# Kernel tuning notes

Measured on AMD Instinct MI355X. Metric: run time of the kernel, lower is better.

## Reference

```python
import jax, jax.numpy as jnp
import numpy as np
import math

E = 1024   # embedding_dim
H = 16     # num_attention_heads
DH = 64    # head_embedding_dim
THD = H * DH
EPS = 1e-5

def _layernorm(x, g, b):
    m = jnp.mean(x, axis=-1, keepdims=True)
    v = jnp.mean(jnp.square(x - m), axis=-1, keepdims=True)
    return (x - m) * jax.lax.rsqrt(v + EPS) * g + b

def setup_inputs() -> dict:
    key = jax.random.key(0)
    ks = jax.random.split(key, 16)
    s_in = 1.0 / math.sqrt(E)
    s_o = 1.0 / math.sqrt(THD)
    inp = {"tokens": jax.random.normal(ks[0], (2, 2048, E), dtype=jnp.float32)}
    # q_linear / k_linear / v_linear: LayerNorm(E) then Linear(E -> THD)
    for i, name in enumerate(["q", "k", "v"]):
        inp[f"ln_{name}_g"] = jnp.ones((E,), jnp.float32)
        inp[f"ln_{name}_b"] = jnp.zeros((E,), jnp.float32)
        inp[f"W{name}"] = jax.random.uniform(ks[1 + 2 * i], (E, THD), jnp.float32, -s_in, s_in)
        inp[f"b{name}"] = jax.random.uniform(ks[2 + 2 * i], (THD,), jnp.float32, -s_in, s_in)
    # attention_linear: LayerNorm(THD) then Linear(THD -> E)
    inp["ln_o_g"] = jnp.ones((THD,), jnp.float32)
    inp["ln_o_b"] = jnp.zeros((THD,), jnp.float32)
    inp["Wo"] = jax.random.uniform(ks[7], (THD, E), jnp.float32, -s_o, s_o)
    inp["bo"] = jax.random.uniform(ks[8], (E,), jnp.float32, -s_o, s_o)
    return inp

def reference(tokens, ln_q_g, ln_q_b, Wq, bq, ln_k_g, ln_k_b, Wk, bk,
              ln_v_g, ln_v_b, Wv, bv, ln_o_g, ln_o_b, Wo, bo):
    N, L, _ = tokens.shape
    # NOTE: faithful to source quirk -- k comes from v_linear, v comes from k_linear.
    q = (_layernorm(tokens, ln_q_g, ln_q_b) @ Wq + bq).reshape(N, L, H, DH).transpose(0, 2, 1, 3)  # (N,H,L,Dh)
    k = (_layernorm(tokens, ln_v_g, ln_v_b) @ Wv + bv).reshape(N, L, H, DH).transpose(0, 2, 3, 1)  # (N,H,Dh,L)
    v = (_layernorm(tokens, ln_k_g, ln_k_b) @ Wk + bk).reshape(N, L, H, DH).transpose(0, 2, 1, 3)  # (N,H,L,Dh)
    qkT = jnp.einsum('bhid,bhdj->bhij', q, k)  # (N,H,L,L)
    # mask added BEFORE dividing by sqrt(Dh), as in source
    mask = jnp.triu(jnp.full((L, L), -9999.0, dtype=qkT.dtype), k=1)
    attn = jax.nn.softmax((qkT + mask) / math.sqrt(DH), axis=-1)
    wv = jnp.einsum('bhij,bhjd->bhid', attn, v).transpose(0, 2, 1, 3).reshape(N, L, THD)
    out = _layernorm(wv, ln_o_g, ln_o_b) @ Wo + bo + tokens
    return (out, k, v)
```

## Files before the change

kernel.cpp:

```cpp
#include <hip/hip_runtime.h>

#define L_SEQ 2048
#define NH    16
#define E_DIM 1024
#define M_ROWS 4096

typedef unsigned short u16;
typedef unsigned int   u32;
typedef __attribute__((ext_vector_type(8))) __bf16 bf16x8;
typedef __attribute__((ext_vector_type(4))) float  f32x4;

__device__ __forceinline__ u16 f2bf(float f) {
  union { float f; u32 u; } x; x.f = f;
  u32 u = x.u;
  return (u16)((u + 0x7FFFu + ((u >> 16) & 1u)) >> 16);
}
__device__ __forceinline__ float bf2f(u16 v) {
  union { u32 u; float f; } x; x.u = ((u32)v) << 16;
  return x.f;
}
__device__ __forceinline__ void st_bf4(u16* p, float a, float b, float c, float d) {
  ushort4 u; u.x = f2bf(a); u.y = f2bf(b); u.z = f2bf(c); u.w = f2bf(d);
  *reinterpret_cast<ushort4*>(p) = u;
}
__device__ __forceinline__ void gload16(const u16* g, u16* l) {
  __builtin_amdgcn_global_load_lds(
      (const __attribute__((address_space(1))) void*)g,
      (__attribute__((address_space(3))) void*)l, 16, 0, 0);
}
#define SBAR() asm volatile("s_barrier" ::: "memory")

__global__ __launch_bounds__(256) void ln_hat_f32(const float* __restrict__ x, u16* __restrict__ o)
{
  __shared__ float red[8];
  const size_t row = blockIdx.x;
  const int t = threadIdx.x;
  float4 v = reinterpret_cast<const float4*>(x + row * E_DIM)[t];
  float s = v.x + v.y + v.z + v.w;
  float q = v.x*v.x + v.y*v.y + v.z*v.z + v.w*v.w;
  #pragma unroll
  for (int off = 32; off; off >>= 1) { s += __shfl_down(s, off); q += __shfl_down(q, off); }
  if ((t & 63) == 0) { red[t >> 6] = s; red[4 + (t >> 6)] = q; }
  __syncthreads();
  float S = red[0] + red[1] + red[2] + red[3];
  float Q = red[4] + red[5] + red[6] + red[7];
  float mean = S * (1.f / E_DIM);
  float rstd = rsqrtf(Q * (1.f / E_DIM) - mean * mean + 1e-5f);
  st_bf4(o + row * E_DIM + t * 4,
         (v.x - mean) * rstd, (v.y - mean) * rstd, (v.z - mean) * rstd, (v.w - mean) * rstd);
}

__global__ __launch_bounds__(256) void ln_hat_bf16(const u16* __restrict__ x, u16* __restrict__ o)
{
  __shared__ float red[8];
  const size_t row = blockIdx.x;
  const int t = threadIdx.x;
  ushort4 u = reinterpret_cast<const ushort4*>(x + row * E_DIM)[t];
  float v0 = bf2f(u.x), v1 = bf2f(u.y), v2 = bf2f(u.z), v3 = bf2f(u.w);
  float s = v0 + v1 + v2 + v3;
  float q = v0*v0 + v1*v1 + v2*v2 + v3*v3;
  #pragma unroll
  for (int off = 32; off; off >>= 1) { s += __shfl_down(s, off); q += __shfl_down(q, off); }
  if ((t & 63) == 0) { red[t >> 6] = s; red[4 + (t >> 6)] = q; }
  __syncthreads();
  float S = red[0] + red[1] + red[2] + red[3];
  float Q = red[4] + red[5] + red[6] + red[7];
  float mean = S * (1.f / E_DIM);
  float rstd = rsqrtf(Q * (1.f / E_DIM) - mean * mean + 1e-5f);
  st_bf4(o + row * E_DIM + t * 4,
         (v0 - mean) * rstd, (v1 - mean) * rstd, (v2 - mean) * rstd, (v3 - mean) * rstd);
}

__global__ __launch_bounds__(256) void transpose_all(
    const float* __restrict__ W0, const float* __restrict__ W1,
    const float* __restrict__ W2, const float* __restrict__ W3,
    const float* __restrict__ g0, const float* __restrict__ g1,
    const float* __restrict__ g2, const float* __restrict__ g3,
    u16* __restrict__ T0, u16* __restrict__ T1, u16* __restrict__ T2, u16* __restrict__ T3)
{
  __shared__ float tile[32][33];
  const int z = blockIdx.z;
  const float* W = (z == 0) ? W0 : (z == 1) ? W1 : (z == 2) ? W2 : W3;
  const float* g = (z == 0) ? g0 : (z == 1) ? g1 : (z == 2) ? g2 : g3;
  u16* T = (z == 0) ? T0 : (z == 1) ? T1 : (z == 2) ? T2 : T3;
  const int tx = threadIdx.x & 31, ty = threadIdx.x >> 5;
  const int bx = blockIdx.x * 32, by = blockIdx.y * 32;
  #pragma unroll
  for (int r = 0; r < 4; ++r) {
    const int e = by + ty + r * 8;
    tile[ty + r * 8][tx] = W[(size_t)e * E_DIM + bx + tx] * g[e];
  }
  __syncthreads();
  #pragma unroll
  for (int r = 0; r < 4; ++r)
    T[(size_t)(bx + ty + r * 8) * E_DIM + by + tx] = f2bf(tile[tx][ty + r * 8]);
}

__global__ __launch_bounds__(256) void bias_fold(
    const float* __restrict__ W0, const float* __restrict__ W1,
    const float* __restrict__ W2, const float* __restrict__ W3,
    const float* __restrict__ l0, const float* __restrict__ l1,
    const float* __restrict__ l2, const float* __restrict__ l3,
    const float* __restrict__ b0, const float* __restrict__ b1,
    const float* __restrict__ b2, const float* __restrict__ b3,
    float* __restrict__ bfold)
{
  __shared__ float part[8][32];
  const int z = blockIdx.y;
  const float* W  = (z == 0) ? W0 : (z == 1) ? W1 : (z == 2) ? W2 : W3;
  const float* bl = (z == 0) ? l0 : (z == 1) ? l1 : (z == 2) ? l2 : l3;
  const float* bs = (z == 0) ? b0 : (z == 1) ? b1 : (z == 2) ? b2 : b3;
  const int tn = threadIdx.x & 31, te = threadIdx.x >> 5;
  const int n = blockIdx.x * 32 + tn;
  float acc = 0.f;
  const int e0 = te * 128;
  for (int e = e0; e < e0 + 128; ++e) acc += bl[e] * W[(size_t)e * E_DIM + n];
  part[te][tn] = acc;
  __syncthreads();
  if (te == 0) {
    float s = part[0][tn] + part[1][tn] + part[2][tn] + part[3][tn]
            + part[4][tn] + part[5][tn] + part[6][tn] + part[7][tn];
    bfold[z * E_DIM + n] = bs[n] + s;
  }
}

#define GBK 64
__device__ __forceinline__ void core128(
    const u16* __restrict__ A, const u16* __restrict__ BT,
    int m0, int n0, int t, u16* lds, f32x4 (&acc)[4][4])
{
  const int lane = t & 63, wave = t >> 6;
  const int wm = wave >> 1, wn = wave & 1;
  const int fr = lane & 15, hi = lane >> 4;
  const int sx = fr & 7;

  auto STAGE = [&](int buf, int kt) {
    u16* la = lds + (buf * 2 + 0) * (128 * GBK);
    u16* lb = lds + (buf * 2 + 1) * (128 * GBK);
    #pragma unroll
    for (int s = 0; s < 4; ++s) {
      const int seg = t + s * 256;
      const int r = seg >> 3;
      const int gc = (seg & 7) ^ (r & 7);
      gload16(A + (size_t)(m0 + r) * E_DIM + kt * GBK + gc * 8, la + seg * 8);
    }
    #pragma unroll
    for (int s = 0; s < 4; ++s) {
      const int seg = t + s * 256;
      const int r = seg >> 3;
      const int gc = (seg & 7) ^ (r & 7);
      gload16(BT + (size_t)(n0 + r) * E_DIM + kt * GBK + gc * 8, lb + seg * 8);
    }
  };
  auto AF = [&](int buf, int i, int ks) -> bf16x8 {
    return *reinterpret_cast<const bf16x8*>(
        lds + (buf * 2 + 0) * (128 * GBK) + (wm * 64 + i * 16 + fr) * GBK + (((ks * 4 + hi) ^ sx) * 8));
  };
  auto BF = [&](int buf, int j, int ks) -> bf16x8 {
    return *reinterpret_cast<const bf16x8*>(
        lds + (buf * 2 + 1) * (128 * GBK) + (wn * 64 + j * 16 + fr) * GBK + (((ks * 4 + hi) ^ sx) * 8));
  };
  auto PHASES = [&](int buf) {
    bf16x8 a[4][2], b[4][2];
    #pragma unroll
    for (int i = 0; i < 4; ++i) { a[i][0] = AF(buf, i, 0); a[i][1] = AF(buf, i, 1); }
    #pragma unroll
    for (int j = 0; j < 4; ++j) { b[j][0] = BF(buf, j, 0); b[j][1] = BF(buf, j, 1); }
    __builtin_amdgcn_s_setprio(1);
    #pragma unroll
    for (int i = 0; i < 4; ++i)
      #pragma unroll
      for (int j = 0; j < 4; ++j) {
        acc[i][j] = __builtin_amdgcn_mfma_f32_16x16x32_bf16(a[i][0], b[j][0], acc[i][j], 0, 0, 0);
        acc[i][j] = __builtin_amdgcn_mfma_f32_16x16x32_bf16(a[i][1], b[j][1], acc[i][j], 0, 0, 0);
      }
    __builtin_amdgcn_s_setprio(0);
  };

  STAGE(0, 0);
  #pragma unroll 1
  for (int kt = 0; kt < 15; ++kt) {
    const int buf = kt & 1;
    SBAR();
    STAGE(buf ^ 1, kt + 1);
    asm volatile("s_waitcnt vmcnt(8)" ::: "memory");
    SBAR();
    PHASES(buf);
  }
  asm volatile("s_waitcnt vmcnt(0)" ::: "memory");
  SBAR();
  PHASES(1);
}

__global__ __launch_bounds__(256, 2) void gemm_qkv128(
    const u16* __restrict__ xhat, const u16* __restrict__ WTcat,
    const float* __restrict__ bfold,
    float* __restrict__ kout, float* __restrict__ vout,
    u16* __restrict__ qbf, u16* __restrict__ kbf, u16* __restrict__ vTb)
{
  __shared__ __align__(16) char smraw[128 * 132 * 4];
  u16* lds = (u16*)smraw;
  const int t = threadIdx.x;
  const int xcd = blockIdx.x & 7, l = blockIdx.x >> 3;
  const int by = 8 * (xcd >> 1) + l / 12;
  const int bx = 12 * (xcd & 1) + l % 12;
  const int m0 = by * 128, n0 = bx * 128;

  f32x4 acc[4][4] = {};
  core128(xhat, WTcat, m0, n0, t, lds, acc);

  const int lane = t & 63, wave = t >> 6;
  const int wm = wave >> 1, wn = wave & 1;
  const int fr = lane & 15, hi = lane >> 4;
  const int z = n0 >> 10;
  const float* bias = bfold + z * E_DIM;
  const int rowb = hi * 4;
  const int bb = m0 >> 11;

  if (z == 0) {
    #pragma unroll
    for (int i = 0; i < 4; ++i) {
      const int mbase = m0 + wm * 64 + i * 16 + rowb;
      #pragma unroll
      for (int j = 0; j < 4; ++j) {
        const int ncol = (n0 + wn * 64 + j * 16 + fr) & 1023;
        const float bval = bias[ncol];
        const int h = ncol >> 6, d = ncol & 63;
        #pragma unroll
        for (int r = 0; r < 4; ++r) {
          const int m = mbase + r;
          const int ltok = m & 2047;
          qbf[(((size_t)(bb * NH + h) * L_SEQ + ltok) << 6) + d] = f2bf(acc[i][j][r] + bval);
        }
      }
    }
  } else if (z == 1) {
    __syncthreads();
    float (*xp)[132] = (float(*)[132])smraw;
    #pragma unroll
    for (int i = 0; i < 4; ++i) {
      const int mbase = m0 + wm * 64 + i * 16 + rowb;
      const int mloc = wm * 64 + i * 16 + rowb;
      #pragma unroll
      for (int j = 0; j < 4; ++j) {
        const int nl = wn * 64 + j * 16 + fr;
        const int ncol = (n0 + nl) & 1023;
        const float bval = bias[ncol];
        const int h = ncol >> 6, d = ncol & 63;
        #pragma unroll
        for (int r = 0; r < 4; ++r) {
          const int m = mbase + r;
          const int ltok = m & 2047;
          const float val = acc[i][j][r] + bval;
          kbf[(((size_t)(bb * NH + h) * L_SEQ + ltok) << 6) + d] = f2bf(val);
          xp[nl][mloc + r] = val;
        }
      }
    }
    __syncthreads();
    const int nl = t >> 1, mh = (t & 1) * 64;
    const int ncol2 = (n0 + nl) & 1023;
    const int h2 = ncol2 >> 6, d2 = ncol2 & 63;
    float4* dst = (float4*)(kout + ((size_t)(bb * NH + h2) * 64 + d2) * L_SEQ + (m0 & 2047) + mh);
    #pragma unroll
    for (int u = 0; u < 16; ++u)
      dst[u] = *reinterpret_cast<float4*>(&xp[nl][mh + u * 4]);
  } else {
    __syncthreads();
    u32 (*vp)[68] = (u32(*)[68])smraw;
    #pragma unroll
    for (int i = 0; i < 4; ++i) {
      const int mbase = m0 + wm * 64 + i * 16 + rowb;
      const int mloc = wm * 64 + i * 16 + rowb;
      #pragma unroll
      for (int j = 0; j < 4; ++j) {
        const int nl = wn * 64 + j * 16 + fr;
        const int ncol = (n0 + nl) & 1023;
        const float bval = bias[ncol];
        const int h = ncol >> 6, d = ncol & 63;
        float v4[4];
        #pragma unroll
        for (int r = 0; r < 4; ++r) {
          const int m = mbase + r;
          const int ltok = m & 2047;
          v4[r] = acc[i][j][r] + bval;
          vout[((size_t)(bb * NH + h) * L_SEQ + ltok) * 64 + d] = v4[r];
        }
        vp[nl][(mloc >> 1) + 0] = (u32)f2bf(v4[0]) | ((u32)f2bf(v4[1]) << 16);
        vp[nl][(mloc >> 1) + 1] = (u32)f2bf(v4[2]) | ((u32)f2bf(v4[3]) << 16);
      }
    }
    __syncthreads();
    const int nl = t >> 1, mh = (t & 1) * 64;
    const int ncol2 = (n0 + nl) & 1023;
    const int h2 = ncol2 >> 6, d2 = ncol2 & 63;
    uint4* dst = (uint4*)(vTb + ((size_t)(bb * NH + h2) * 64 + d2) * L_SEQ + (m0 & 2047) + mh);
    #pragma unroll
    for (int u = 0; u < 8; ++u)
      dst[u] = *reinterpret_cast<uint4*>(&vp[nl][(mh >> 1) + u * 4]);
  }
}

__global__ __launch_bounds__(256, 2) void gemm_o128(
    const u16* __restrict__ A, const u16* __restrict__ BT, const float* __restrict__ bias,
    const float* __restrict__ tokens, float* __restrict__ out)
{
  __shared__ u16 lds[4 * 128 * GBK];
  const int t = threadIdx.x;
  const int xcd = blockIdx.x & 7, l = blockIdx.x >> 3;
  const int by = 8 * (xcd >> 1) + (l >> 2);
  const int bx = 4 * (xcd & 1) + (l & 3);
  const int m0 = by * 128, n0 = bx * 128;

  f32x4 acc[4][4] = {};
  core128(A, BT, m0, n0, t, lds, acc);

  const int lane = t & 63, wave = t >> 6;
  const int wm = wave >> 1, wn = wave & 1;
  const int fr = lane & 15, hi = lane >> 4;
  const int rowb = hi * 4;
  #pragma unroll
  for (int i = 0; i < 4; ++i) {
    const int mbase = m0 + wm * 64 + i * 16 + rowb;
    #pragma unroll
    for (int j = 0; j < 4; ++j) {
      const int ncol = n0 + wn * 64 + j * 16 + fr;
      const float bval = bias[ncol];
      #pragma unroll
      for (int r = 0; r < 4; ++r) {
        const int m = mbase + r;
        out[(size_t)m * E_DIM + ncol] = acc[i][j][r] + bval + tokens[(size_t)m * E_DIM + ncol];
      }
    }
  }
}

__global__ __launch_bounds__(256) void attn_mfma(
    const u16* __restrict__ qbf, const u16* __restrict__ kbf,
    const u16* __restrict__ vTb, u16* __restrict__ wv)
{
  __shared__ u16 Klds[64][72];
  __shared__ u16 Vlds[64][72];
  __shared__ u16 Plds[4][16][72];
  const int t = threadIdx.x, lane = t & 63, wave = t >> 6;
  const int bi = blockIdx.x;
  const int bh = (bi & 7) + 8 * ((bi >> 3) & 3);
  const int pr = bi >> 5;
  const int fr = lane & 15, hi = lane >> 4;
  const u16* kbase = kbf + (size_t)bh * L_SEQ * 64;
  const u16* vbase = vTb + (size_t)bh * 64 * L_SEQ;
  const int b = bh >> 4, h = bh & 15;

  #pragma unroll 1
  for (int half = 0; half < 2; ++half) {
    const int qt = half ? (31 - pr) : pr;
    const int q0w = qt * 64 + wave * 16;
    const int qg = q0w + fr;

    const u16* qrow = qbf + ((size_t)bh * L_SEQ + q0w + fr) * 64 + hi * 8;
    const bf16x8 qf0 = *reinterpret_cast<const bf16x8*>(qrow);
    const bf16x8 qf1 = *reinterpret_cast<const bf16x8*>(qrow + 32);

    f32x4 o[4] = {};
    float mrun = -3.0e38f, lrun = 0.f;

    for (int tkv = 0; tkv <= qt; ++tkv) {
      const int j0 = tkv * 64;
      const bool diag = (tkv == qt);
      #pragma unroll
      for (int s = 0; s < 2; ++s) {
        const int seg = t + s * 256;
        const int r = seg >> 3, c8 = (seg & 7) * 8;
        *reinterpret_cast<uint4*>(&Klds[r][c8]) =
            *reinterpret_cast<const uint4*>(kbase + (size_t)(j0 + r) * 64 + c8);
        *reinterpret_cast<uint4*>(&Vlds[r][c8]) =
            *reinterpret_cast<const uint4*>(vbase + (size_t)r * L_SEQ + j0 + c8);
      }
      __syncthreads();

      f32x4 st[4] = {};
      __builtin_amdgcn_s_setprio(1);
      #pragma unroll
      for (int kt = 0; kt < 4; ++kt) {
        bf16x8 ka0 = *reinterpret_cast<const bf16x8*>(&Klds[kt*16 + fr][hi*8]);
        bf16x8 ka1 = *reinterpret_cast<const bf16x8*>(&Klds[kt*16 + fr][32 + hi*8]);
        st[kt] = __builtin_amdgcn_mfma_f32_16x16x32_bf16(ka0, qf0, st[kt], 0, 0, 0);
        st[kt] = __builtin_amdgcn_mfma_f32_16x16x32_bf16(ka1, qf1, st[kt], 0, 0, 0);
      }
      __builtin_amdgcn_s_setprio(0);

      float p[16];
      float pmax = -3.0e38f;
      #pragma unroll
      for (int kt = 0; kt < 4; ++kt)
        #pragma unroll
        for (int r = 0; r < 4; ++r) {
          const int key = j0 + kt*16 + hi*4 + r;
          const float v = st[kt][r] * 0.125f +
                          ((diag && key > qg) ? -1249.875f : 0.f);
          p[kt*4 + r] = v;
          pmax = fmaxf(pmax, v);
        }
      pmax = fmaxf(pmax, __shfl_xor(pmax, 16));
      pmax = fmaxf(pmax, __shfl_xor(pmax, 32));
      const float mnew = fmaxf(mrun, pmax);
      const float alpha = __expf(mrun - mnew);
      float lsum = 0.f;
      #pragma unroll
      for (int i = 0; i < 16; ++i) { p[i] = __expf(p[i] - mnew); lsum += p[i]; }
      lsum += __shfl_xor(lsum, 16);
      lsum += __shfl_xor(lsum, 32);
      lrun = lrun * alpha + lsum;
      mrun = mnew;
      #pragma unroll
      for (int r = 0; r < 4; ++r) {
        const float ar = __shfl(alpha, hi*4 + r);
        o[0][r] *= ar; o[1][r] *= ar; o[2][r] *= ar; o[3][r] *= ar;
      }

      #pragma unroll
      for (int kt = 0; kt < 4; ++kt) {
        ushort4 w4;
        w4.x = f2bf(p[kt*4+0]); w4.y = f2bf(p[kt*4+1]);
        w4.z = f2bf(p[kt*4+2]); w4.w = f2bf(p[kt*4+3]);
        *reinterpret_cast<ushort4*>(&Plds[wave][fr][kt*16 + hi*4]) = w4;
      }

      const bf16x8 pf0 = *reinterpret_cast<const bf16x8*>(&Plds[wave][fr][hi*8]);
      const bf16x8 pf1 = *reinterpret_cast<const bf16x8*>(&Plds[wave][fr][32 + hi*8]);
      __builtin_amdgcn_s_setprio(1);
      #pragma unroll
      for (int dt = 0; dt < 4; ++dt) {
        bf16x8 vf0 = *reinterpret_cast<const bf16x8*>(&Vlds[dt*16 + fr][hi*8]);
        bf16x8 vf1 = *reinterpret_cast<const bf16x8*>(&Vlds[dt*16 + fr][32 + hi*8]);
        o[dt] = __builtin_amdgcn_mfma_f32_16x16x32_bf16(pf0, vf0, o[dt], 0, 0, 0);
        o[dt] = __builtin_amdgcn_mfma_f32_16x16x32_bf16(pf1, vf1, o[dt], 0, 0, 0);
      }
      __builtin_amdgcn_s_setprio(0);
      __syncthreads();
    }

    const float inv = 1.f / lrun;
    #pragma unroll
    for (int r = 0; r < 4; ++r) {
      const float ir = __shfl(inv, hi*4 + r);
      const int q = q0w + hi*4 + r;
      u16* dst = wv + (size_t)(b * L_SEQ + q) * E_DIM + h * 64 + fr;
      #pragma unroll
      for (int dt = 0; dt < 4; ++dt)
        dst[dt * 16] = f2bf(o[dt][r] * ir);
    }
  }
}

extern "C" void kernel_launch(void* const* d_in, const int* in_sizes, int n_in,
                              void* d_out, int out_size, void* d_ws, size_t ws_size,
                              hipStream_t stream) {
  (void)in_sizes; (void)n_in; (void)out_size; (void)ws_size;
  const float* tokens = (const float*)d_in[0];
  const float* ln_q_g = (const float*)d_in[1];
  const float* ln_q_b = (const float*)d_in[2];
  const float* Wq     = (const float*)d_in[3];
  const float* bq     = (const float*)d_in[4];
  const float* ln_k_g = (const float*)d_in[5];
  const float* ln_k_b = (const float*)d_in[6];
  const float* Wk     = (const float*)d_in[7];
  const float* bk     = (const float*)d_in[8];
  const float* ln_v_g = (const float*)d_in[9];
  const float* ln_v_b = (const float*)d_in[10];
  const float* Wv     = (const float*)d_in[11];
  const float* bv     = (const float*)d_in[12];
  const float* ln_o_g = (const float*)d_in[13];
  const float* ln_o_b = (const float*)d_in[14];
  const float* Wo     = (const float*)d_in[15];
  const float* bo     = (const float*)d_in[16];

  float* out  = (float*)d_out;
  float* kout = out + 4194304;
  float* vout = kout + 4194304;

  char* w = (char*)d_ws;
  const size_t MB = (size_t)1 << 20;
  u16*   WTq   = (u16*)(w + 0 * MB);
  u16*   WTv   = (u16*)(w + 2 * MB);
  u16*   WTk   = (u16*)(w + 4 * MB);
  u16*   WTo   = (u16*)(w + 6 * MB);
  u16*   xhat  = (u16*)(w + 8 * MB);
  u16*   qbf   = (u16*)(w + 16 * MB);
  u16*   kbf   = (u16*)(w + 24 * MB);
  u16*   vTb   = (u16*)(w + 32 * MB);
  u16*   what  = (u16*)(w + 40 * MB);
  float* bfold = (float*)(w + 48 * MB);
  u16*   wvb   = xhat;

  transpose_all<<<dim3(32, 32, 4), 256, 0, stream>>>(
      Wq, Wv, Wk, Wo, ln_q_g, ln_v_g, ln_k_g, ln_o_g, WTq, WTv, WTk, WTo);
  bias_fold<<<dim3(32, 4), 256, 0, stream>>>(
      Wq, Wv, Wk, Wo, ln_q_b, ln_v_b, ln_k_b, ln_o_b, bq, bv, bk, bo, bfold);
  ln_hat_f32<<<M_ROWS, 256, 0, stream>>>(tokens, xhat);
  gemm_qkv128<<<768, 256, 0, stream>>>(xhat, WTq, bfold, kout, vout, qbf, kbf, vTb);
  attn_mfma<<<512, 256, 0, stream>>>(qbf, kbf, vTb, wvb);
  ln_hat_bf16<<<M_ROWS, 256, 0, stream>>>(wvb, what);
  gemm_o128<<<256, 256, 0, stream>>>(what, WTo, bfold + 3 * E_DIM, tokens, out);
}
```

Measured before the change: 129.8 us.

## Split causal attention KV range across two blocks and merge partials

Adds a split-KV attention kernel that launches twice as many blocks. Each pair of blocks shares the long query tile's KV range: one block covers tiles 0-16, the other covers the rest and then also handles the short query tile. Partial outputs plus running max and sum go to workspace and are merged by a new combine kernel. The aim is better load balance and more occupancy on the many-CU device, at the cost of an extra launch and fp32 partial traffic. It runs only when the workspace is large enough.

```diff
diff --git a/kernel.cpp b/kernel.cpp
--- a/kernel.cpp
+++ b/kernel.cpp
@@ -335,6 +335,183 @@
   }
 }
 
+__global__ __launch_bounds__(256, 4) void attn_split(
+    const u16* __restrict__ qbf, const u16* __restrict__ kbf,
+    const u16* __restrict__ vTb, u16* __restrict__ wv,
+    float* __restrict__ po, float* __restrict__ pml)
+{
+  __shared__ u16 Klds[64][72];
+  __shared__ u16 Vlds[64][72];
+  __shared__ u16 Plds[4][16][72];
+  const int t = threadIdx.x, lane = t & 63, wave = t >> 6;
+  const int bi = blockIdx.x;
+  const int bh = (bi & 7) + 8 * ((bi >> 3) & 3);
+  const int pp = bi >> 5;
+  const int half = pp & 1, pr = pp >> 1;
+  const int fr = lane & 15, hi = lane >> 4;
+  const u16* kbase = kbf + (size_t)bh * L_SEQ * 64;
+  const u16* vbase = vTb + (size_t)bh * 64 * L_SEQ;
+  const int b = bh >> 4, h = bh & 15;
+  const int qtA = 31 - pr, qtB = pr;
+
+  auto STG = [&](int j0) {
+    #pragma unroll
+    for (int s = 0; s < 2; ++s) {
+      const int seg = t + s * 256;
+      const int r = seg >> 3, c8 = (seg & 7) * 8;
+      *reinterpret_cast<uint4*>(&Klds[r][c8]) =
+          *reinterpret_cast<const uint4*>(kbase + (size_t)(j0 + r) * 64 + c8);
+      *reinterpret_cast<uint4*>(&Vlds[r][c8]) =
+          *reinterpret_cast<const uint4*>(vbase + (size_t)r * L_SEQ + j0 + c8);
+    }
+  };
+  auto TILE = [&](const bf16x8& qf0, const bf16x8& qf1, int qg, bool diag, int j0,
+                  f32x4 (&o)[4], float& mrun, float& lrun) {
+    f32x4 st[4] = {};
+    __builtin_amdgcn_s_setprio(1);
+    #pragma unroll
+    for (int kt = 0; kt < 4; ++kt) {
+      bf16x8 ka0 = *reinterpret_cast<const bf16x8*>(&Klds[kt*16 + fr][hi*8]);
+      bf16x8 ka1 = *reinterpret_cast<const bf16x8*>(&Klds[kt*16 + fr][32 + hi*8]);
+      st[kt] = __builtin_amdgcn_mfma_f32_16x16x32_bf16(ka0, qf0, st[kt], 0, 0, 0);
+      st[kt] = __builtin_amdgcn_mfma_f32_16x16x32_bf16(ka1, qf1, st[kt], 0, 0, 0);
+    }
+    __builtin_amdgcn_s_setprio(0);
+
+    float p[16];
+    float pmax = -3.0e38f;
+    #pragma unroll
+    for (int kt = 0; kt < 4; ++kt)
+      #pragma unroll
+      for (int r = 0; r < 4; ++r) {
+        const int key = j0 + kt*16 + hi*4 + r;
+        const float v = st[kt][r] * 0.125f + ((diag && key > qg) ? -1249.875f : 0.f);
+        p[kt*4 + r] = v;
+        pmax = fmaxf(pmax, v);
+      }
+    pmax = fmaxf(pmax, __shfl_xor(pmax, 16));
+    pmax = fmaxf(pmax, __shfl_xor(pmax, 32));
+    const float mnew = fmaxf(mrun, pmax);
+    const float alpha = __expf(mrun - mnew);
+    float lsum = 0.f;
+    #pragma unroll
+    for (int i = 0; i < 16; ++i) { p[i] = __expf(p[i] - mnew); lsum += p[i]; }
+    lsum += __shfl_xor(lsum, 16);
+    lsum += __shfl_xor(lsum, 32);
+    lrun = lrun * alpha + lsum;
+    mrun = mnew;
+    #pragma unroll
+    for (int r = 0; r < 4; ++r) {
+      const float ar = __shfl(alpha, hi*4 + r);
+      o[0][r] *= ar; o[1][r] *= ar; o[2][r] *= ar; o[3][r] *= ar;
+    }
+    #pragma unroll
+    for (int kt = 0; kt < 4; ++kt) {
+      ushort4 w4;
+      w4.x = f2bf(p[kt*4+0]); w4.y = f2bf(p[kt*4+1]);
+      w4.z = f2bf(p[kt*4+2]); w4.w = f2bf(p[kt*4+3]);
+      *reinterpret_cast<ushort4*>(&Plds[wave][fr][kt*16 + hi*4]) = w4;
+    }
+    const bf16x8 pf0 = *reinterpret_cast<const bf16x8*>(&Plds[wave][fr][hi*8]);
+    const bf16x8 pf1 = *reinterpret_cast<const bf16x8*>(&Plds[wave][fr][32 + hi*8]);
+    __builtin_amdgcn_s_setprio(1);
+    #pragma unroll
+    for (int dt = 0; dt < 4; ++dt) {
+      bf16x8 vf0 = *reinterpret_cast<const bf16x8*>(&Vlds[dt*16 + fr][hi*8]);
+      bf16x8 vf1 = *reinterpret_cast<const bf16x8*>(&Vlds[dt*16 + fr][32 + hi*8]);
+      o[dt] = __builtin_amdgcn_mfma_f32_16x16x32_bf16(pf0, vf0, o[dt], 0, 0, 0);
+      o[dt] = __builtin_amdgcn_mfma_f32_16x16x32_bf16(pf1, vf1, o[dt], 0, 0, 0);
+    }
+    __builtin_amdgcn_s_setprio(0);
+  };
+
+  {
+    const int q0w = qtA * 64 + wave * 16;
+    const int qg = q0w + fr;
+    const u16* qrow = qbf + ((size_t)bh * L_SEQ + q0w + fr) * 64 + hi * 8;
+    const bf16x8 qf0 = *reinterpret_cast<const bf16x8*>(qrow);
+    const bf16x8 qf1 = *reinterpret_cast<const bf16x8*>(qrow + 32);
+    f32x4 o[4] = {};
+    float mrun = -3.0e38f, lrun = 0.f;
+    const int lo = half ? 17 : 0;
+    const int hiT = half ? qtA : 16;
+    #pragma unroll 1
+    for (int tkv = lo; tkv <= hiT; ++tkv) {
+      STG(tkv * 64);
+      __syncthreads();
+      TILE(qf0, qf1, qg, tkv == qtA, tkv * 64, o, mrun, lrun);
+      __syncthreads();
+    }
+    const int slot = (bh * 16 + pr) * 2 + half;
+    float* pob = po + (size_t)slot * 4096;
+    #pragma unroll
+    for (int dt = 0; dt < 4; ++dt)
+      #pragma unroll
+      for (int r = 0; r < 4; ++r)
+        pob[(wave * 16 + hi * 4 + r) * 64 + dt * 16 + fr] = o[dt][r];
+    if (hi == 0) {
+      pml[slot * 128 + wave * 16 + fr] = mrun;
+      pml[slot * 128 + 64 + wave * 16 + fr] = lrun;
+    }
+  }
+
+  if (half) {
+    const int q0w = qtB * 64 + wave * 16;
+    const int qg = q0w + fr;
+    const u16* qrow = qbf + ((size_t)bh * L_SEQ + q0w + fr) * 64 + hi * 8;
+    const bf16x8 qf0 = *reinterpret_cast<const bf16x8*>(qrow);
+    const bf16x8 qf1 = *reinterpret_cast<const bf16x8*>(qrow + 32);
+    f32x4 o[4] = {};
+    float mrun = -3.0e38f, lrun = 0.f;
+    #pragma unroll 1
+    for (int tkv = 0; tkv <= qtB; ++tkv) {
+      __syncthreads();
+      STG(tkv * 64);
+      __syncthreads();
+      TILE(qf0, qf1, qg, tkv == qtB, tkv * 64, o, mrun, lrun);
+    }
+    const float inv = 1.f / lrun;
+    #pragma unroll
+    for (int r = 0; r < 4; ++r) {
+      const float ir = __shfl(inv, hi * 4 + r);
+      const int q = q0w + hi * 4 + r;
+      u16* dst = wv + (size_t)(b * L_SEQ + q) * E_DIM + h * 64 + fr;
+      #pragma unroll
+      for (int dt = 0; dt < 4; ++dt)
+        dst[dt * 16] = f2bf(o[dt][r] * ir);
+    }
+  }
+}
+
+__global__ __launch_bounds__(256) void attn_combine(
+    const float* __restrict__ po, const float* __restrict__ pml, u16* __restrict__ wv)
+{
+  const int pair = blockIdx.x;
+  const int bh = pair >> 4, pr = pair & 15;
+  const int b = bh >> 4, h = bh & 15;
+  const int q0 = (31 - pr) * 64;
+  const int t = threadIdx.x;
+  const int r = t >> 2, c0 = (t & 3) * 16;
+  const float m0 = pml[(size_t)(pair * 2 + 0) * 128 + r];
+  const float l0 = pml[(size_t)(pair * 2 + 0) * 128 + 64 + r];
+  const float m1 = pml[(size_t)(pair * 2 + 1) * 128 + r];
+  const float l1 = pml[(size_t)(pair * 2 + 1) * 128 + 64 + r];
+  const float mm = fmaxf(m0, m1);
+  const float a0 = __expf(m0 - mm), a1 = __expf(m1 - mm);
+  const float inv = 1.f / (l0 * a0 + l1 * a1);
+  const float* o0 = po + ((size_t)(pair * 2 + 0) * 64 + r) * 64 + c0;
+  const float* o1 = po + ((size_t)(pair * 2 + 1) * 64 + r) * 64 + c0;
+  u16* dst = wv + (size_t)(b * L_SEQ + q0 + r) * E_DIM + h * 64 + c0;
+  #pragma unroll
+  for (int c = 0; c < 16; c += 4) {
+    float4 x0 = *reinterpret_cast<const float4*>(o0 + c);
+    float4 x1 = *reinterpret_cast<const float4*>(o1 + c);
+    st_bf4(dst + c,
+           (x0.x * a0 + x1.x * a1) * inv, (x0.y * a0 + x1.y * a1) * inv,
+           (x0.z * a0 + x1.z * a1) * inv, (x0.w * a0 + x1.w * a1) * inv);
+  }
+}
+
 __global__ __launch_bounds__(256) void attn_mfma(
     const u16* __restrict__ qbf, const u16* __restrict__ kbf,
     const u16* __restrict__ vTb, u16* __restrict__ wv)
@@ -356,11 +533,9 @@
     const int qt = half ? (31 - pr) : pr;
     const int q0w = qt * 64 + wave * 16;
     const int qg = q0w + fr;
-
     const u16* qrow = qbf + ((size_t)bh * L_SEQ + q0w + fr) * 64 + hi * 8;
     const bf16x8 qf0 = *reinterpret_cast<const bf16x8*>(qrow);
     const bf16x8 qf1 = *reinterpret_cast<const bf16x8*>(qrow + 32);
-
     f32x4 o[4] = {};
     float mrun = -3.0e38f, lrun = 0.f;
 
@@ -396,8 +571,7 @@
         #pragma unroll
         for (int r = 0; r < 4; ++r) {
           const int key = j0 + kt*16 + hi*4 + r;
-          const float v = st[kt][r] * 0.125f +
-                          ((diag && key > qg) ? -1249.875f : 0.f);
+          const float v = st[kt][r] * 0.125f + ((diag && key > qg) ? -1249.875f : 0.f);
           p[kt*4 + r] = v;
           pmax = fmaxf(pmax, v);
         }
@@ -417,7 +591,6 @@
         const float ar = __shfl(alpha, hi*4 + r);
         o[0][r] *= ar; o[1][r] *= ar; o[2][r] *= ar; o[3][r] *= ar;
       }
-
       #pragma unroll
       for (int kt = 0; kt < 4; ++kt) {
         ushort4 w4;
@@ -425,7 +598,6 @@
         w4.z = f2bf(p[kt*4+2]); w4.w = f2bf(p[kt*4+3]);
         *reinterpret_cast<ushort4*>(&Plds[wave][fr][kt*16 + hi*4]) = w4;
       }
-
       const bf16x8 pf0 = *reinterpret_cast<const bf16x8*>(&Plds[wave][fr][hi*8]);
       const bf16x8 pf1 = *reinterpret_cast<const bf16x8*>(&Plds[wave][fr][32 + hi*8]);
       __builtin_amdgcn_s_setprio(1);
@@ -456,7 +628,7 @@
 extern "C" void kernel_launch(void* const* d_in, const int* in_sizes, int n_in,
                               void* d_out, int out_size, void* d_ws, size_t ws_size,
                               hipStream_t stream) {
-  (void)in_sizes; (void)n_in; (void)out_size; (void)ws_size;
+  (void)in_sizes; (void)n_in; (void)out_size;
   const float* tokens = (const float*)d_in[0];
   const float* ln_q_g = (const float*)d_in[1];
   const float* ln_q_b = (const float*)d_in[2];
@@ -491,6 +663,8 @@
   u16*   vTb   = (u16*)(w + 32 * MB);
   u16*   what  = (u16*)(w + 40 * MB);
   float* bfold = (float*)(w + 48 * MB);
+  float* po    = (float*)(w + 49 * MB);
+  float* pml   = (float*)(w + 65 * MB);
   u16*   wvb   = xhat;
 
   transpose_all<<<dim3(32, 32, 4), 256, 0, stream>>>(
@@ -499,7 +673,12 @@
       Wq, Wv, Wk, Wo, ln_q_b, ln_v_b, ln_k_b, ln_o_b, bq, bv, bk, bo, bfold);
   ln_hat_f32<<<M_ROWS, 256, 0, stream>>>(tokens, xhat);
   gemm_qkv128<<<768, 256, 0, stream>>>(xhat, WTq, bfold, kout, vout, qbf, kbf, vTb);
-  attn_mfma<<<512, 256, 0, stream>>>(qbf, kbf, vTb, wvb);
+  if (ws_size >= 66 * MB) {
+    attn_split<<<1024, 256, 0, stream>>>(qbf, kbf, vTb, wvb, po, pml);
+    attn_combine<<<512, 256, 0, stream>>>(po, pml, wvb);
+  } else {
+    attn_mfma<<<512, 256, 0, stream>>>(qbf, kbf, vTb, wvb);
+  }
   ln_hat_bf16<<<M_ROWS, 256, 0, stream>>>(wvb, what);
   gemm_o128<<<256, 256, 0, stream>>>(what, WTo, bfold + 3 * E_DIM, tokens, out);
 }
```

Result: no change. 129.5 us (-0.2%).

## Split long attention rows across blocks, read K/V directly, fuse prep kernels

Applied to the files above, without the earlier changes.

Fuses the weight transpose, bias fold and input layernorm into one prep kernel launch. Attention now splits the long causal query tiles across two blocks (split-KV), writing fp32 partial outputs plus running max and sum, and the output layernorm kernel merges them. The attention kernel drops its shared-memory K/V staging and loads MFMA fragments straight from global memory, with no per-tile barriers and a 4-block occupancy hint. The aim is better load balance, more parallelism and fewer launches, at the cost of extra partial-result traffic and uncoalesced, unshared global K/V reads.

```diff
diff --git a/kernel.cpp b/kernel.cpp
--- a/kernel.cpp
+++ b/kernel.cpp
@@ -30,33 +30,112 @@
 }
 #define SBAR() asm volatile("s_barrier" ::: "memory")
 
-__global__ __launch_bounds__(256) void ln_hat_f32(const float* __restrict__ x, u16* __restrict__ o)
+__global__ __launch_bounds__(256) void prep_kernel(
+    const float* __restrict__ tokens,
+    const float* __restrict__ W0, const float* __restrict__ W1,
+    const float* __restrict__ W2, const float* __restrict__ W3,
+    const float* __restrict__ g0, const float* __restrict__ g1,
+    const float* __restrict__ g2, const float* __restrict__ g3,
+    const float* __restrict__ lb0, const float* __restrict__ lb1,
+    const float* __restrict__ lb2, const float* __restrict__ lb3,
+    const float* __restrict__ bs0, const float* __restrict__ bs1,
+    const float* __restrict__ bs2, const float* __restrict__ bs3,
+    u16* __restrict__ T0, u16* __restrict__ T1, u16* __restrict__ T2, u16* __restrict__ T3,
+    float* __restrict__ bfold, u16* __restrict__ xhat)
+{
+  __shared__ __align__(16) float shm[32 * 33];
+  const int bid = blockIdx.x;
+  const int t = threadIdx.x;
+
+  if (bid < 4096) {
+    const int z = bid >> 10, rem = bid & 1023;
+    const float* W = (z == 0) ? W0 : (z == 1) ? W1 : (z == 2) ? W2 : W3;
+    const float* g = (z == 0) ? g0 : (z == 1) ? g1 : (z == 2) ? g2 : g3;
+    u16* T = (z == 0) ? T0 : (z == 1) ? T1 : (z == 2) ? T2 : T3;
+    float (*tile)[33] = (float(*)[33])shm;
+    const int tx = t & 31, ty = t >> 5;
+    const int bx = (rem & 31) * 32, by = (rem >> 5) * 32;
+    #pragma unroll
+    for (int r = 0; r < 4; ++r) {
+      const int e = by + ty + r * 8;
+      tile[ty + r * 8][tx] = W[(size_t)e * E_DIM + bx + tx] * g[e];
+    }
+    __syncthreads();
+    #pragma unroll
+    for (int r = 0; r < 4; ++r)
+      T[(size_t)(bx + ty + r * 8) * E_DIM + by + tx] = f2bf(tile[tx][ty + r * 8]);
+  } else if (bid < 4224) {
+    const int idx = bid - 4096;
+    const int z = idx >> 5;
+    const float* W  = (z == 0) ? W0 : (z == 1) ? W1 : (z == 2) ? W2 : W3;
+    const float* bl = (z == 0) ? lb0 : (z == 1) ? lb1 : (z == 2) ? lb2 : lb3;
+    const float* bs = (z == 0) ? bs0 : (z == 1) ? bs1 : (z == 2) ? bs2 : bs3;
+    float (*part)[32] = (float(*)[32])shm;
+    const int tn = t & 31, te = t >> 5;
+    const int n = (idx & 31) * 32 + tn;
+    float acc = 0.f;
+    const int e0 = te * 128;
+    for (int e = e0; e < e0 + 128; ++e) acc += bl[e] * W[(size_t)e * E_DIM + n];
+    part[te][tn] = acc;
+    __syncthreads();
+    if (te == 0) {
+      float s = part[0][tn] + part[1][tn] + part[2][tn] + part[3][tn]
+              + part[4][tn] + part[5][tn] + part[6][tn] + part[7][tn];
+      bfold[z * E_DIM + n] = bs[n] + s;
+    }
+  } else {
+    float* red = shm;
+    const size_t row = bid - 4224;
+    float4 v = reinterpret_cast<const float4*>(tokens + row * E_DIM)[t];
+    float s = v.x + v.y + v.z + v.w;
+    float q = v.x*v.x + v.y*v.y + v.z*v.z + v.w*v.w;
+    #pragma unroll
+    for (int off = 32; off; off >>= 1) { s += __shfl_down(s, off); q += __shfl_down(q, off); }
+    if ((t & 63) == 0) { red[t >> 6] = s; red[4 + (t >> 6)] = q; }
+    __syncthreads();
+    float S = red[0] + red[1] + red[2] + red[3];
+    float Q = red[4] + red[5] + red[6] + red[7];
+    float mean = S * (1.f / E_DIM);
+    float rstd = rsqrtf(Q * (1.f / E_DIM) - mean * mean + 1e-5f);
+    st_bf4(xhat + row * E_DIM + t * 4,
+           (v.x - mean) * rstd, (v.y - mean) * rstd, (v.z - mean) * rstd, (v.w - mean) * rstd);
+  }
+}
+
+__global__ __launch_bounds__(256) void ln_combine_hat(
+    const u16* __restrict__ wvb, const float* __restrict__ po,
+    const float* __restrict__ pml, u16* __restrict__ what)
 {
   __shared__ float red[8];
-  const size_t row = blockIdx.x;
+  const int row = blockIdx.x;
   const int t = threadIdx.x;
-  float4 v = reinterpret_cast<const float4*>(x + row * E_DIM)[t];
-  float s = v.x + v.y + v.z + v.w;
-  float q = v.x*v.x + v.y*v.y + v.z*v.z + v.w*v.w;
-  #pragma unroll
-  for (int off = 32; off; off >>= 1) { s += __shfl_down(s, off); q += __shfl_down(q, off); }
-  if ((t & 63) == 0) { red[t >> 6] = s; red[4 + (t >> 6)] = q; }
-  __syncthreads();
-  float S = red[0] + red[1] + red[2] + red[3];
-  float Q = red[4] + red[5] + red[6] + red[7];
-  float mean = S * (1.f / E_DIM);
-  float rstd = rsqrtf(Q * (1.f / E_DIM) - mean * mean + 1e-5f);
-  st_bf4(o + row * E_DIM + t * 4,
-         (v.x - mean) * rstd, (v.y - mean) * rstd, (v.z - mean) * rstd, (v.w - mean) * rstd);
-}
-
-__global__ __launch_bounds__(256) void ln_hat_bf16(const u16* __restrict__ x, u16* __restrict__ o)
-{
-  __shared__ float red[8];
-  const size_t row = blockIdx.x;
-  const int t = threadIdx.x;
-  ushort4 u = reinterpret_cast<const ushort4*>(x + row * E_DIM)[t];
-  float v0 = bf2f(u.x), v1 = bf2f(u.y), v2 = bf2f(u.z), v3 = bf2f(u.w);
+  const int l = row & (L_SEQ - 1), b = row >> 11;
+  const int qt = l >> 6;
+  float v0, v1, v2, v3;
+  if (qt >= 16) {
+    const int pr = 31 - qt;
+    const int c = t * 4;
+    const int h = c >> 6, d0 = c & 63;
+    const int bh = b * NH + h;
+    const int base = (bh * 16 + pr) * 2;
+    const int rr = l & 63;
+    const float m0 = pml[(size_t)base * 128 + rr];
+    const float s0 = pml[(size_t)base * 128 + 64 + rr];
+    const float m1 = pml[(size_t)(base + 1) * 128 + rr];
+    const float s1 = pml[(size_t)(base + 1) * 128 + 64 + rr];
+    const float mm = fmaxf(m0, m1);
+    const float a0 = __expf(m0 - mm), a1 = __expf(m1 - mm);
+    const float inv = 1.f / (s0 * a0 + s1 * a1);
+    float4 x0 = *reinterpret_cast<const float4*>(po + ((size_t)base * 64 + rr) * 64 + d0);
+    float4 x1 = *reinterpret_cast<const float4*>(po + ((size_t)(base + 1) * 64 + rr) * 64 + d0);
+    v0 = (x0.x * a0 + x1.x * a1) * inv;
+    v1 = (x0.y * a0 + x1.y * a1) * inv;
+    v2 = (x0.z * a0 + x1.z * a1) * inv;
+    v3 = (x0.w * a0 + x1.w * a1) * inv;
+  } else {
+    ushort4 u = reinterpret_cast<const ushort4*>(wvb + (size_t)row * E_DIM)[t];
+    v0 = bf2f(u.x); v1 = bf2f(u.y); v2 = bf2f(u.z); v3 = bf2f(u.w);
+  }
   float s = v0 + v1 + v2 + v3;
   float q = v0*v0 + v1*v1 + v2*v2 + v3*v3;
   #pragma unroll
@@ -67,61 +146,8 @@
   float Q = red[4] + red[5] + red[6] + red[7];
   float mean = S * (1.f / E_DIM);
   float rstd = rsqrtf(Q * (1.f / E_DIM) - mean * mean + 1e-5f);
-  st_bf4(o + row * E_DIM + t * 4,
+  st_bf4(what + (size_t)row * E_DIM + t * 4,
          (v0 - mean) * rstd, (v1 - mean) * rstd, (v2 - mean) * rstd, (v3 - mean) * rstd);
-}
-
-__global__ __launch_bounds__(256) void transpose_all(
-    const float* __restrict__ W0, const float* __restrict__ W1,
-    const float* __restrict__ W2, const float* __restrict__ W3,
-    const float* __restrict__ g0, const float* __restrict__ g1,
-    const float* __restrict__ g2, const float* __restrict__ g3,
-    u16* __restrict__ T0, u16* __restrict__ T1, u16* __restrict__ T2, u16* __restrict__ T3)
-{
-  __shared__ float tile[32][33];
-  const int z = blockIdx.z;
-  const float* W = (z == 0) ? W0 : (z == 1) ? W1 : (z == 2) ? W2 : W3;
-  const float* g = (z == 0) ? g0 : (z == 1) ? g1 : (z == 2) ? g2 : g3;
-  u16* T = (z == 0) ? T0 : (z == 1) ? T1 : (z == 2) ? T2 : T3;
-  const int tx = threadIdx.x & 31, ty = threadIdx.x >> 5;
-  const int bx = blockIdx.x * 32, by = blockIdx.y * 32;
-  #pragma unroll
-  for (int r = 0; r < 4; ++r) {
-    const int e = by + ty + r * 8;
-    tile[ty + r * 8][tx] = W[(size_t)e * E_DIM + bx + tx] * g[e];
-  }
-  __syncthreads();
-  #pragma unroll
-  for (int r = 0; r < 4; ++r)
-    T[(size_t)(bx + ty + r * 8) * E_DIM + by + tx] = f2bf(tile[tx][ty + r * 8]);
-}
-
-__global__ __launch_bounds__(256) void bias_fold(
-    const float* __restrict__ W0, const float* __restrict__ W1,
-    const float* __restrict__ W2, const float* __restrict__ W3,
-    const float* __restrict__ l0, const float* __restrict__ l1,
-    const float* __restrict__ l2, const float* __restrict__ l3,
-    const float* __restrict__ b0, const float* __restrict__ b1,
-    const float* __restrict__ b2, const float* __restrict__ b3,
-    float* __restrict__ bfold)
-{
-  __shared__ float part[8][32];
-  const int z = blockIdx.y;
-  const float* W  = (z == 0) ? W0 : (z == 1) ? W1 : (z == 2) ? W2 : W3;
-  const float* bl = (z == 0) ? l0 : (z == 1) ? l1 : (z == 2) ? l2 : l3;
-  const float* bs = (z == 0) ? b0 : (z == 1) ? b1 : (z == 2) ? b2 : b3;
-  const int tn = threadIdx.x & 31, te = threadIdx.x >> 5;
-  const int n = blockIdx.x * 32 + tn;
-  float acc = 0.f;
-  const int e0 = te * 128;
-  for (int e = e0; e < e0 + 128; ++e) acc += bl[e] * W[(size_t)e * E_DIM + n];
-  part[te][tn] = acc;
-  __syncthreads();
-  if (te == 0) {
-    float s = part[0][tn] + part[1][tn] + part[2][tn] + part[3][tn]
-            + part[4][tn] + part[5][tn] + part[6][tn] + part[7][tn];
-    bfold[z * E_DIM + n] = bs[n] + s;
-  }
 }
 
 #define GBK 64
@@ -335,116 +361,127 @@
   }
 }
 
-__global__ __launch_bounds__(256) void attn_mfma(
+__global__ __launch_bounds__(256, 4) void attn_direct(
     const u16* __restrict__ qbf, const u16* __restrict__ kbf,
-    const u16* __restrict__ vTb, u16* __restrict__ wv)
+    const u16* __restrict__ vTb, u16* __restrict__ wv,
+    float* __restrict__ po, float* __restrict__ pml)
 {
-  __shared__ u16 Klds[64][72];
-  __shared__ u16 Vlds[64][72];
   __shared__ u16 Plds[4][16][72];
   const int t = threadIdx.x, lane = t & 63, wave = t >> 6;
   const int bi = blockIdx.x;
   const int bh = (bi & 7) + 8 * ((bi >> 3) & 3);
-  const int pr = bi >> 5;
+  const int pp = bi >> 5;
+  const int half = pp & 1, pr = pp >> 1;
   const int fr = lane & 15, hi = lane >> 4;
-  const u16* kbase = kbf + (size_t)bh * L_SEQ * 64;
-  const u16* vbase = vTb + (size_t)bh * 64 * L_SEQ;
   const int b = bh >> 4, h = bh & 15;
-
-  #pragma unroll 1
-  for (int half = 0; half < 2; ++half) {
-    const int qt = half ? (31 - pr) : pr;
-    const int q0w = qt * 64 + wave * 16;
+  const int qtA = 31 - pr, qtB = pr;
+  const u16* kfrag = kbf + (size_t)bh * L_SEQ * 64 + (size_t)fr * 64 + hi * 8;
+  const u16* vfrag = vTb + (size_t)bh * 64 * L_SEQ + (size_t)fr * L_SEQ + hi * 8;
+
+  auto TILE = [&](const bf16x8& qf0, const bf16x8& qf1, int qg, bool diag, int j0,
+                  f32x4 (&o)[4], float& mrun, float& lrun) {
+    f32x4 st[4] = {};
+    __builtin_amdgcn_s_setprio(1);
+    #pragma unroll
+    for (int kt = 0; kt < 4; ++kt) {
+      const u16* kp = kfrag + (size_t)(j0 + kt * 16) * 64;
+      bf16x8 ka0 = *reinterpret_cast<const bf16x8*>(kp);
+      bf16x8 ka1 = *reinterpret_cast<const bf16x8*>(kp + 32);
+      st[kt] = __builtin_amdgcn_mfma_f32_16x16x32_bf16(ka0, qf0, st[kt], 0, 0, 0);
+      st[kt] = __builtin_amdgcn_mfma_f32_16x16x32_bf16(ka1, qf1, st[kt], 0, 0, 0);
+    }
+    __builtin_amdgcn_s_setprio(0);
+
+    float p[16];
+    float pmax = -3.0e38f;
+    #pragma unroll
+    for (int kt = 0; kt < 4; ++kt)
+      #pragma unroll
+      for (int r = 0; r < 4; ++r) {
+        const int key = j0 + kt*16 + hi*4 + r;
+        const float v = st[kt][r] * 0.125f + ((diag && key > qg) ? -1249.875f : 0.f);
+        p[kt*4 + r] = v;
+        pmax = fmaxf(pmax, v);
+      }
+    pmax = fmaxf(pmax, __shfl_xor(pmax, 16));
+    pmax = fmaxf(pmax, __shfl_xor(pmax, 32));
+    const float mnew = fmaxf(mrun, pmax);
+    const float alpha = __expf(mrun - mnew);
+    float lsum = 0.f;
+    #pragma unroll
+    for (int i = 0; i < 16; ++i) { p[i] = __expf(p[i] - mnew); lsum += p[i]; }
+    lsum += __shfl_xor(lsum, 16);
+    lsum += __shfl_xor(lsum, 32);
+    lrun = lrun * alpha + lsum;
+    mrun = mnew;
+    #pragma unroll
+    for (int r = 0; r < 4; ++r) {
+      const float ar = __shfl(alpha, hi*4 + r);
+      o[0][r] *= ar; o[1][r] *= ar; o[2][r] *= ar; o[3][r] *= ar;
+    }
+    #pragma unroll
+    for (int kt = 0; kt < 4; ++kt) {
+      ushort4 w4;
+      w4.x = f2bf(p[kt*4+0]); w4.y = f2bf(p[kt*4+1]);
+      w4.z = f2bf(p[kt*4+2]); w4.w = f2bf(p[kt*4+3]);
+      *reinterpret_cast<ushort4*>(&Plds[wave][fr][kt*16 + hi*4]) = w4;
+    }
+    const bf16x8 pf0 = *reinterpret_cast<const bf16x8*>(&Plds[wave][fr][hi*8]);
+    const bf16x8 pf1 = *reinterpret_cast<const bf16x8*>(&Plds[wave][fr][32 + hi*8]);
+    __builtin_amdgcn_s_setprio(1);
+    #pragma unroll
+    for (int dt = 0; dt < 4; ++dt) {
+      const u16* vp = vfrag + (size_t)(dt * 16) * L_SEQ + j0;
+      bf16x8 vf0 = *reinterpret_cast<const bf16x8*>(vp);
+      bf16x8 vf1 = *reinterpret_cast<const bf16x8*>(vp + 32);
+      o[dt] = __builtin_amdgcn_mfma_f32_16x16x32_bf16(pf0, vf0, o[dt], 0, 0, 0);
+      o[dt] = __builtin_amdgcn_mfma_f32_16x16x32_bf16(pf1, vf1, o[dt], 0, 0, 0);
+    }
+    __builtin_amdgcn_s_setprio(0);
+  };
+
+  {
+    const int q0w = qtA * 64 + wave * 16;
     const int qg = q0w + fr;
-
     const u16* qrow = qbf + ((size_t)bh * L_SEQ + q0w + fr) * 64 + hi * 8;
     const bf16x8 qf0 = *reinterpret_cast<const bf16x8*>(qrow);
     const bf16x8 qf1 = *reinterpret_cast<const bf16x8*>(qrow + 32);
-
     f32x4 o[4] = {};
     float mrun = -3.0e38f, lrun = 0.f;
-
-    for (int tkv = 0; tkv <= qt; ++tkv) {
-      const int j0 = tkv * 64;
-      const bool diag = (tkv == qt);
-      #pragma unroll
-      for (int s = 0; s < 2; ++s) {
-        const int seg = t + s * 256;
-        const int r = seg >> 3, c8 = (seg & 7) * 8;
-        *reinterpret_cast<uint4*>(&Klds[r][c8]) =
-            *reinterpret_cast<const uint4*>(kbase + (size_t)(j0 + r) * 64 + c8);
-        *reinterpret_cast<uint4*>(&Vlds[r][c8]) =
-            *reinterpret_cast<const uint4*>(vbase + (size_t)r * L_SEQ + j0 + c8);
-      }
-      __syncthreads();
-
-      f32x4 st[4] = {};
-      __builtin_amdgcn_s_setprio(1);
-      #pragma unroll
-      for (int kt = 0; kt < 4; ++kt) {
-        bf16x8 ka0 = *reinterpret_cast<const bf16x8*>(&Klds[kt*16 + fr][hi*8]);
-        bf16x8 ka1 = *reinterpret_cast<const bf16x8*>(&Klds[kt*16 + fr][32 + hi*8]);
-        st[kt] = __builtin_amdgcn_mfma_f32_16x16x32_bf16(ka0, qf0, st[kt], 0, 0, 0);
-        st[kt] = __builtin_amdgcn_mfma_f32_16x16x32_bf16(ka1, qf1, st[kt], 0, 0, 0);
-      }
-      __builtin_amdgcn_s_setprio(0);
-
-      float p[16];
-      float pmax = -3.0e38f;
-      #pragma unroll
-      for (int kt = 0; kt < 4; ++kt)
-        #pragma unroll
-        for (int r = 0; r < 4; ++r) {
-          const int key = j0 + kt*16 + hi*4 + r;
-          const float v = st[kt][r] * 0.125f +
-                          ((diag && key > qg) ? -1249.875f : 0.f);
-          p[kt*4 + r] = v;
-          pmax = fmaxf(pmax, v);
-        }
-      pmax = fmaxf(pmax, __shfl_xor(pmax, 16));
-      pmax = fmaxf(pmax, __shfl_xor(pmax, 32));
-      const float mnew = fmaxf(mrun, pmax);
-      const float alpha = __expf(mrun - mnew);
-      float lsum = 0.f;
-      #pragma unroll
-      for (int i = 0; i < 16; ++i) { p[i] = __expf(p[i] - mnew); lsum += p[i]; }
-      lsum += __shfl_xor(lsum, 16);
-      lsum += __shfl_xor(lsum, 32);
-      lrun = lrun * alpha + lsum;
-      mrun = mnew;
-      #pragma unroll
-      for (int r = 0; r < 4; ++r) {
-        const float ar = __shfl(alpha, hi*4 + r);
-        o[0][r] *= ar; o[1][r] *= ar; o[2][r] *= ar; o[3][r] *= ar;
-      }
-
-      #pragma unroll
-      for (int kt = 0; kt < 4; ++kt) {
-        ushort4 w4;
-        w4.x = f2bf(p[kt*4+0]); w4.y = f2bf(p[kt*4+1]);
-        w4.z = f2bf(p[kt*4+2]); w4.w = f2bf(p[kt*4+3]);
-        *reinterpret_cast<ushort4*>(&Plds[wave][fr][kt*16 + hi*4]) = w4;
-      }
-
-      const bf16x8 pf0 = *reinterpret_cast<const bf16x8*>(&Plds[wave][fr][hi*8]);
-      const bf16x8 pf1 = *reinterpret_cast<const bf16x8*>(&Plds[wave][fr][32 + hi*8]);
-      __builtin_amdgcn_s_setprio(1);
-      #pragma unroll
-      for (int dt = 0; dt < 4; ++dt) {
-        bf16x8 vf0 = *reinterpret_cast<const bf16x8*>(&Vlds[dt*16 + fr][hi*8]);
-        bf16x8 vf1 = *reinterpret_cast<const bf16x8*>(&Vlds[dt*16 + fr][32 + hi*8]);
-        o[dt] = __builtin_amdgcn_mfma_f32_16x16x32_bf16(pf0, vf0, o[dt], 0, 0, 0);
-        o[dt] = __builtin_amdgcn_mfma_f32_16x16x32_bf16(pf1, vf1, o[dt], 0, 0, 0);
-      }
-      __builtin_amdgcn_s_setprio(0);
-      __syncthreads();
-    }
-
+    const int lo = half ? 17 : 0;
+    const int hiT = half ? qtA : 16;
+    #pragma unroll 1
+    for (int tkv = lo; tkv <= hiT; ++tkv)
+      TILE(qf0, qf1, qg, tkv == qtA, tkv * 64, o, mrun, lrun);
+    const int slot = (bh * 16 + pr) * 2 + half;
+    float* pob = po + (size_t)slot * 4096;
+    #pragma unroll
+    for (int dt = 0; dt < 4; ++dt)
+      #pragma unroll
+      for (int r = 0; r < 4; ++r)
+        pob[(wave * 16 + hi * 4 + r) * 64 + dt * 16 + fr] = o[dt][r];
+    if (hi == 0) {
+      pml[slot * 128 + wave * 16 + fr] = mrun;
+      pml[slot * 128 + 64 + wave * 16 + fr] = lrun;
+    }
+  }
+
+  if (half) {
+    const int q0w = qtB * 64 + wave * 16;
+    const int qg = q0w + fr;
+    const u16* qrow = qbf + ((size_t)bh * L_SEQ + q0w + fr) * 64 + hi * 8;
+    const bf16x8 qf0 = *reinterpret_cast<const bf16x8*>(qrow);
+    const bf16x8 qf1 = *reinterpret_cast<const bf16x8*>(qrow + 32);
+    f32x4 o[4] = {};
+    float mrun = -3.0e38f, lrun = 0.f;
+    #pragma unroll 1
+    for (int tkv = 0; tkv <= qtB; ++tkv)
+      TILE(qf0, qf1, qg, tkv == qtB, tkv * 64, o, mrun, lrun);
     const float inv = 1.f / lrun;
     #pragma unroll
     for (int r = 0; r < 4; ++r) {
-      const float ir = __shfl(inv, hi*4 + r);
-      const int q = q0w + hi*4 + r;
+      const float ir = __shfl(inv, hi * 4 + r);
+      const int q = q0w + hi * 4 + r;
       u16* dst = wv + (size_t)(b * L_SEQ + q) * E_DIM + h * 64 + fr;
       #pragma unroll
       for (int dt = 0; dt < 4; ++dt)
@@ -491,15 +528,19 @@
   u16*   vTb   = (u16*)(w + 32 * MB);
   u16*   what  = (u16*)(w + 40 * MB);
   float* bfold = (float*)(w + 48 * MB);
+  float* po    = (float*)(w + 49 * MB);
+  float* pml   = (float*)(w + 65 * MB);
   u16*   wvb   = xhat;
 
-  transpose_all<<<dim3(32, 32, 4), 256, 0, stream>>>(
-      Wq, Wv, Wk, Wo, ln_q_g, ln_v_g, ln_k_g, ln_o_g, WTq, WTv, WTk, WTo);
-  bias_fold<<<dim3(32, 4), 256, 0, stream>>>(
-      Wq, Wv, Wk, Wo, ln_q_b, ln_v_b, ln_k_b, ln_o_b, bq, bv, bk, bo, bfold);
-  ln_hat_f32<<<M_ROWS, 256, 0, stream>>>(tokens, xhat);
+  prep_kernel<<<8320, 256, 0, stream>>>(
+      tokens,
+      Wq, Wv, Wk, Wo,
+      ln_q_g, ln_v_g, ln_k_g, ln_o_g,
+      ln_q_b, ln_v_b, ln_k_b, ln_o_b,
+      bq, bv, bk, bo,
+      WTq, WTv, WTk, WTo, bfold, xhat);
   gemm_qkv128<<<768, 256, 0, stream>>>(xhat, WTq, bfold, kout, vout, qbf, kbf, vTb);
-  attn_mfma<<<512, 256, 0, stream>>>(qbf, kbf, vTb, wvb);
-  ln_hat_bf16<<<M_ROWS, 256, 0, stream>>>(wvb, what);
+  attn_direct<<<1024, 256, 0, stream>>>(qbf, kbf, vTb, wvb, po, pml);
+  ln_combine_hat<<<M_ROWS, 256, 0, stream>>>(wvb, po, pml, what);
   gemm_o128<<<256, 256, 0, stream>>>(what, WTo, bfold + 3 * E_DIM, tokens, out);
 }
```

Result: slower. 200.7 us (+54.7%).
